# Optimization experiments

Hardware: AMD Instinct MI355X
Metric: run time of the kernel (lower is better)

## Reference

```python
import jax, jax.numpy as jnp
import numpy as np
import math

F_DIM = 256      # feature_dims
NHEADS = 4
KEY_D = 64
VAL_D = 64
ITERS = 6        # update_iters
N_ATOMS = 100000
N_BONDS = 200000
NEI = 6
ATOM_FDIM = 31
BOND_FDIM = 37   # 31 + 6
NEG_SLOPE = 0.1


def setup_inputs() -> dict:
    key = jax.random.key(0)
    ks = jax.random.split(key, 13)
    s = 0.05
    return {
        "fatoms": jax.random.normal(ks[0], (N_ATOMS, ATOM_FDIM), jnp.float32),
        "fbonds": jax.random.normal(ks[1], (N_BONDS, BOND_FDIM), jnp.float32),
        "agraph": jax.random.randint(ks[2], (N_ATOMS, NEI), 0, N_BONDS),
        "bgraph": jax.random.randint(ks[3], (N_BONDS, NEI), 0, N_BONDS),
        "lig_scope": jax.random.randint(ks[4], (64, 2), 0, N_ATOMS),
        "W_emb": jax.random.normal(ks[5], (BOND_FDIM, F_DIM), jnp.float32) * s,
        "b_emb": jnp.zeros((F_DIM,), jnp.float32),
        "Wq": jax.random.normal(ks[6], (F_DIM, NHEADS * KEY_D), jnp.float32) * s,
        "Wk": jax.random.normal(ks[7], (F_DIM, NHEADS * KEY_D), jnp.float32) * s,
        "Wv": jax.random.normal(ks[8], (F_DIM, NHEADS * VAL_D), jnp.float32) * s,
        "Wout": jax.random.normal(ks[9], (VAL_D, F_DIM), jnp.float32) * s,
        "W_last": jax.random.normal(ks[10], (ATOM_FDIM + F_DIM, F_DIM), jnp.float32) * s,
        "b_last": jnp.zeros((F_DIM,), jnp.float32),
    }


def reference(fatoms, fbonds, agraph, bgraph, lig_scope,
              W_emb, b_emb, Wq, Wk, Wv, Wout, W_last, b_last):
    # Bond embedding + initial message
    fbonds_input = fbonds @ W_emb + b_emb                      # [B, F]
    message = jax.nn.leaky_relu(fbonds_input, NEG_SLOPE)
    # index 0 is the padding bond -> masked out in attention
    nei_mask = jnp.where(bgraph != 0, 0.0, -1e7)[:, None, :]   # [B, 1, NEI]
    inv_sqrt_kd = 1.0 / math.sqrt(KEY_D)

    for _ in range(ITERS - 1):
        nei = message[bgraph]                                  # [B, NEI, F] gather
        q = (message @ Wq).reshape(N_BONDS, NHEADS, KEY_D)     # [B, H, K]
        k = (nei @ Wk).reshape(N_BONDS, NEI, NHEADS, KEY_D)    # [B, NEI, H, K]
        v = (nei @ Wv).reshape(N_BONDS, NEI, NHEADS, VAL_D)    # [B, NEI, H, V]
        scores = jnp.einsum('bhk,bnhk->bhn', q, k) * inv_sqrt_kd + nei_mask
        attn = jax.nn.softmax(scores, axis=-1)                 # [B, H, NEI]
        out = jnp.einsum('bhn,bnhv->bhv', attn, v)             # [B, H, V]
        out = out.mean(axis=1)                                 # mean over heads -> [B, V]
        message = jax.nn.leaky_relu(fbonds_input + out @ Wout, NEG_SLOPE)

    # Aggregate incoming bond messages per atom (index 0 acts as padding row)
    nei_sum = message[agraph].sum(axis=1)                      # [A, F]
    h = jnp.concatenate([fatoms, nei_sum], axis=-1) @ W_last + b_last
    return jax.nn.leaky_relu(h, NEG_SLOPE)
```

## Files before the change

kernel.cpp:

```cpp
#include <hip/hip_runtime.h>

#define N_ATOMS 100000
#define N_BONDS 200000
#define NEI 6
#define ITERS 6

#define MB_PAD 200064
#define MT_B 1563
#define MT_Q 3126
#define MT_A 782
#define KL 320
#define KVSTRIDE 768
#define QSTR 260
#define AUX_NT 2

typedef __bf16 bf16x8 __attribute__((ext_vector_type(8)));
typedef float f32x4 __attribute__((ext_vector_type(4)));
typedef float f32x2 __attribute__((ext_vector_type(2)));

__device__ __forceinline__ float b2f(unsigned short u) {
  union { unsigned int i; float f; } x; x.i = ((unsigned int)u) << 16; return x.f;
}
__device__ __forceinline__ unsigned short f2b(float f) {
  union { float f; unsigned int i; } x; x.f = f;
  unsigned int r = (x.i + 0x7FFFu + ((x.i >> 16) & 1u)) >> 16;
  return (unsigned short)r;
}
__device__ __forceinline__ float lrelu(float v) { return v > 0.f ? v : 0.1f * v; }

#if defined(__has_builtin)
#  if __has_builtin(__builtin_amdgcn_cvt_f32_fp8) && __has_builtin(__builtin_amdgcn_cvt_pk_fp8_f32)
#    define HW_FP8 1
#  endif
#  if __has_builtin(__builtin_amdgcn_cvt_pk_f32_fp8)
#    define HW_PKFP8 1
#  endif
#endif

__device__ __forceinline__ unsigned char f2e4m3_sw(float f) {
  union { float f; unsigned u; } x; x.f = f;
  unsigned s = (x.u >> 24) & 0x80u;
  unsigned ax = x.u & 0x7FFFFFFFu;
  if (ax >= 0x43E00000u) return (unsigned char)(s | 0x7Eu);
  if (ax < 0x3A800000u)  return (unsigned char)s;
  if (ax < 0x3C800000u) {
    union { unsigned u; float f; } a; a.u = ax;
    unsigned n = (unsigned)(a.f * 512.0f + 0.5f);
    return (unsigned char)(s | n);
  }
  unsigned r = ax + 0x0007FFFFu + ((ax >> 20) & 1u);
  unsigned e32 = r >> 23;
  unsigned mant = (r >> 20) & 7u;
  int e8 = (int)e32 - 120;
  if (e8 >= 16) return (unsigned char)(s | 0x7Eu);
  return (unsigned char)(s | ((unsigned)e8 << 3) | mant);
}
__device__ __forceinline__ float dec8_sw(unsigned b) {
  unsigned s = (b & 0x80u) << 24;
  unsigned e = (b >> 3) & 0xFu, m = b & 7u;
  if (e) { union { unsigned u; float f; } x; x.u = s | ((e + 120u) << 23) | (m << 20); return x.f; }
  float v = (float)m * 0.001953125f;
  return (b & 0x80u) ? -v : v;
}
#ifdef HW_FP8
__device__ __forceinline__ unsigned char f2e4m3(float f) {
  return (unsigned char)(__builtin_amdgcn_cvt_pk_fp8_f32(f, f, 0, false) & 0xFF);
}
#define DEC0(x) __builtin_amdgcn_cvt_f32_fp8((int)(x), 0)
#define DEC1(x) __builtin_amdgcn_cvt_f32_fp8((int)(x), 1)
#define DEC2(x) __builtin_amdgcn_cvt_f32_fp8((int)(x), 2)
#define DEC3(x) __builtin_amdgcn_cvt_f32_fp8((int)(x), 3)
#else
__device__ __forceinline__ unsigned char f2e4m3(float f) { return f2e4m3_sw(f); }
#define DEC0(x) dec8_sw((x) & 0xFFu)
#define DEC1(x) dec8_sw(((x) >> 8) & 0xFFu)
#define DEC2(x) dec8_sw(((x) >> 16) & 0xFFu)
#define DEC3(x) dec8_sw(((x) >> 24) & 0xFFu)
#endif

__device__ __forceinline__ int kswz(int k, int n) {
  return (k & ~63) | ((k & 63) ^ ((n & 7) << 3));
}

__global__ __launch_bounds__(256) void pack_weights(
    const float* __restrict__ Wq, const float* __restrict__ Wk,
    const float* __restrict__ Wv, const float* __restrict__ Wemb,
    const float* __restrict__ Wout, const float* __restrict__ Wlast,
    unsigned short* __restrict__ wkvT, unsigned short* __restrict__ wqT,
    unsigned short* __restrict__ wmsgT, unsigned short* __restrict__ wlastT)
{
  int t = blockIdx.x * 256 + threadIdx.x;
  {
    int n = t >> 8, k = t & 255;
    wkvT[n * 256 + kswz(k, n)] =
        f2b((n < 256) ? Wk[k * 256 + n] : Wv[k * 256 + (n - 256)]);
  }
  if (t < 65536) {
    int n = t >> 8, k = t & 255;
    wqT[n * 256 + kswz(k, n)] = f2b(Wq[k * 256 + n]);
  }
  if (t < 32768) {
    int n = t >> 7, k = t & 127;
    float v = 0.f;
    if (k < 64)       v = Wout[k * 256 + n];
    else if (k < 101) v = Wemb[(k - 64) * 256 + n];
    wmsgT[n * 128 + kswz(k, n)] = f2b(v);
  }
  if (t < 256 * KL) {
    int n = t / KL, k = t % KL;
    float v = 0.f;
    if (k < 256)      v = Wlast[(31 + k) * 256 + n];
    else if (k < 287) v = Wlast[(k - 256) * 256 + n];
    wlastT[n * KL + kswz(k, n)] = f2b(v);
  }
}

__global__ __launch_bounds__(256) void pack_bonds(
    const float* __restrict__ fbonds, unsigned short* __restrict__ A2)
{
  int t = blockIdx.x * 256 + threadIdx.x;
  int r = t >> 7, c = t & 127;
  float v = 0.f;
  if (c >= 64 && c < 101 && r < N_BONDS) v = fbonds[r * 37 + (c - 64)];
  A2[t] = f2b(v);
}

template<int EP>
__global__ __launch_bounds__(256) void gemm_bt(
    const unsigned short* __restrict__ A,
    const unsigned short* __restrict__ BT,
    unsigned short* __restrict__ C0,
    float* __restrict__ Fout,
    const float* __restrict__ Xf,
    int K, int N, int Mreal)
{
  __shared__ __align__(16) unsigned short As[128 * 64];
  __shared__ __align__(16) unsigned short Bs[128 * 64];
  const int tid  = threadIdx.x;
  const int wave = tid >> 6, lane = tid & 63;
  const int wr = wave >> 1, wc = wave & 1;
  const int lhi = lane >> 4, llo = lane & 15;
  const int mBase = blockIdx.y * 128;
  const int nBase = blockIdx.x * 128;
  const int crow = tid >> 3, ccol = tid & 7;

  f32x4 acc[4][4];
  #pragma unroll
  for (int i = 0; i < 4; ++i)
    #pragma unroll
    for (int j = 0; j < 4; ++j)
      acc[i][j] = f32x4{0.f, 0.f, 0.f, 0.f};

  for (int k0 = 0; k0 < K; k0 += 64) {
    __syncthreads();
    #pragma unroll
    for (int r = 0; r < 4; ++r) {
      const unsigned short* ga =
          A + (size_t)(mBase + r * 32 + crow) * K + (k0 + ccol * 8);
      __builtin_amdgcn_global_load_lds(
          (const __attribute__((address_space(1))) void*)ga,
          (__attribute__((address_space(3))) void*)(As + r * 2048 + wave * 512), 16, 0, 0);
      const unsigned short* gb =
          BT + (size_t)(nBase + r * 32 + crow) * K + (k0 + ccol * 8);
      __builtin_amdgcn_global_load_lds(
          (const __attribute__((address_space(1))) void*)gb,
          (__attribute__((address_space(3))) void*)(Bs + r * 2048 + wave * 512), 16, 0, 0);
    }
    __syncthreads();
    #pragma unroll
    for (int ks = 0; ks < 2; ++ks) {
      bf16x8 af[4], bfv[4];
      #pragma unroll
      for (int i = 0; i < 4; ++i)
        af[i] = *reinterpret_cast<const bf16x8*>(&As[(wr * 64 + i * 16 + llo) * 64 + ks * 32 + lhi * 8]);
      #pragma unroll
      for (int j = 0; j < 4; ++j)
        bfv[j] = *reinterpret_cast<const bf16x8*>(
            &Bs[(wc * 64 + j * 16 + llo) * 64 + ((ks * 32 + lhi * 8) ^ ((llo & 7) << 3))]);
      #pragma unroll
      for (int i = 0; i < 4; ++i)
        #pragma unroll
        for (int j = 0; j < 4; ++j)
          acc[i][j] = __builtin_amdgcn_mfma_f32_16x16x32_bf16(af[i], bfv[j], acc[i][j], 0, 0, 0);
    }
  }

  #pragma unroll
  for (int i = 0; i < 4; ++i) {
    #pragma unroll
    for (int j = 0; j < 4; ++j) {
      const int col = nBase + wc * 64 + j * 16 + llo;
      #pragma unroll
      for (int r = 0; r < 4; ++r) {
        const int row = mBase + wr * 64 + i * 16 + lhi * 4 + r;
        const float v = acc[i][j][r];
        if (EP == 0) {
          C0[(size_t)row * N + col] = f2b(v);
        } else if (EP == 1) {
          C0[(size_t)row * N + col] = f2b(lrelu(v + Xf[col]));
        } else if (EP == 3) {
          if (row < Mreal) Fout[(size_t)row * N + col] = lrelu(v + Xf[col]);
        } else {
          unsigned char* kvb = (unsigned char*)C0;
          if (nBase < 256) {
            kvb[(size_t)row * KVSTRIDE + col] = f2e4m3(v);
          } else {
            *(unsigned short*)(kvb + (size_t)row * KVSTRIDE + 256 +
                               (size_t)(col - 256) * 2) = f2b(v);
          }
        }
      }
    }
  }
}

#ifdef HW_PKFP8
#define QKDOT(p_, kd_) do {                                                    \
    const f32x2 lo_ = __builtin_amdgcn_cvt_pk_f32_fp8((int)(kd_), false);      \
    const f32x2 hi_ = __builtin_amdgcn_cvt_pk_f32_fp8((int)(kd_), true);       \
    p_ = q0 * lo_.x + q1 * lo_.y + q2 * hi_.x + q3 * hi_.y;                    \
  } while (0)
#else
#define QKDOT(p_, kd_) do {                                                    \
    p_ = q0 * DEC0(kd_) + q1 * DEC1(kd_) + q2 * DEC2(kd_) + q3 * DEC3(kd_);    \
  } while (0)
#endif

#define NLOAD(P, N_)                                                           \
    const int bn##P##N_ = __builtin_amdgcn_readfirstlane(                      \
        bgraph[(size_t)uw##P * NEI + N_]);                                     \
    const unsigned char* bp##P##N_ =                                           \
        kv + (size_t)(unsigned)bn##P##N_ * KVSTRIDE;                           \
    const unsigned kd##P##N_ =                                                 \
        *reinterpret_cast<const unsigned*>(bp##P##N_ + lane * 4);              \
    const ushort4 vu##P##N_ =                                                  \
        *reinterpret_cast<const ushort4*>(bp##P##N_ + 256 + lane * 8);

#define GATHER(P, BL)                                                          \
    const int bl##P = (BL);                                                    \
    const int uw##P = __builtin_amdgcn_readfirstlane(mBase + bl##P);           \
    NLOAD(P, 0) NLOAD(P, 1) NLOAD(P, 2) NLOAD(P, 3) NLOAD(P, 4) NLOAD(P, 5)

#define NSCORE(P, N_)                                                          \
    float sc##P##N_;                                                           \
    {                                                                          \
      float p_;                                                                \
      QKDOT(p_, kd##P##N_);                                                    \
      p_ += __shfl_xor(p_, 1); p_ += __shfl_xor(p_, 2);                        \
      p_ += __shfl_xor(p_, 4); p_ += __shfl_xor(p_, 8);                        \
      sc##P##N_ = p_ * SCL + (bn##P##N_ != 0 ? 0.f : -1e7f);                   \
    }

#define NPV(P, N_)                                                             \
    {                                                                          \
      const float e_ = exp2f(sc##P##N_ - m_);                                  \
      s_ += e_;                                                                \
      o0_ += e_ * b2f(vu##P##N_.x); o1_ += e_ * b2f(vu##P##N_.y);              \
      o2_ += e_ * b2f(vu##P##N_.z); o3_ += e_ * b2f(vu##P##N_.w);              \
    }

#define COMPUTE(P)                                                             \
    {                                                                          \
      const ushort4 qu_ = *reinterpret_cast<const ushort4*>(                   \
          &smem[bl##P * QSTR + lane * 4]);                                     \
      const float q0 = b2f(qu_.x), q1 = b2f(qu_.y);                            \
      const float q2 = b2f(qu_.z), q3 = b2f(qu_.w);                            \
      NSCORE(P, 0) NSCORE(P, 1) NSCORE(P, 2)                                   \
      NSCORE(P, 3) NSCORE(P, 4) NSCORE(P, 5)                                   \
      const float m_ =                                                         \
          fmaxf(fmaxf(fmaxf(sc##P##0, sc##P##1), fmaxf(sc##P##2, sc##P##3)),   \
                fmaxf(sc##P##4, sc##P##5));                                    \
      float s_ = 0.f, o0_ = 0.f, o1_ = 0.f, o2_ = 0.f, o3_ = 0.f;              \
      NPV(P, 0) NPV(P, 1) NPV(P, 2) NPV(P, 3) NPV(P, 4) NPV(P, 5)              \
      const float inv_ = 0.25f * __builtin_amdgcn_rcpf(s_);                    \
      o0_ *= inv_; o1_ *= inv_; o2_ *= inv_; o3_ *= inv_;                      \
      o0_ += __shfl_xor(o0_, 16); o0_ += __shfl_xor(o0_, 32);                  \
      o1_ += __shfl_xor(o1_, 16); o1_ += __shfl_xor(o1_, 32);                  \
      o2_ += __shfl_xor(o2_, 16); o2_ += __shfl_xor(o2_, 32);                  \
      o3_ += __shfl_xor(o3_, 16); o3_ += __shfl_xor(o3_, 32);                  \
      if (lane < 16) {                                                         \
        ushort4 ov_;                                                           \
        ov_.x = f2b(o0_); ov_.y = f2b(o1_);                                    \
        ov_.z = f2b(o2_); ov_.w = f2b(o3_);                                    \
        *reinterpret_cast<ushort4*>(                                           \
            A2 + (size_t)(mBase + bl##P) * 128 + lane * 4) = ov_;              \
      }                                                                        \
    }

__global__ __launch_bounds__(512, 6) void fused_qattn(
    const unsigned short* __restrict__ msg,
    const unsigned short* __restrict__ wqT,
    const unsigned char* __restrict__ kv,
    const int* __restrict__ bgraph,
    unsigned short* __restrict__ A2)
{
  __shared__ __align__(16) unsigned short smem[20480];
  const int tid  = threadIdx.x;
  const int wave = tid >> 6, lane = tid & 63;
  const int wr = wave >> 2, wc = wave & 3;
  const int lhi = lane >> 4, llo = lane & 15;
  const int mBase = blockIdx.x * 64;
  const int crow = tid >> 3, ccol = tid & 7;

  f32x4 acc[2][4];
  #pragma unroll
  for (int i = 0; i < 2; ++i)
    #pragma unroll
    for (int j = 0; j < 4; ++j)
      acc[i][j] = f32x4{0.f, 0.f, 0.f, 0.f};

  for (int k0 = 0; k0 < 256; k0 += 64) {
    __syncthreads();
    {
      const unsigned short* ga =
          msg + (size_t)(mBase + crow) * 256 + (k0 + ccol * 8);
      __builtin_amdgcn_global_load_lds(
          (const __attribute__((address_space(1))) void*)ga,
          (__attribute__((address_space(3))) void*)(smem + wave * 512), 16, 0, AUX_NT);
    }
    #pragma unroll
    for (int r = 0; r < 4; ++r) {
      const unsigned short* gb =
          wqT + (size_t)(r * 64 + crow) * 256 + (k0 + ccol * 8);
      __builtin_amdgcn_global_load_lds(
          (const __attribute__((address_space(1))) void*)gb,
          (__attribute__((address_space(3))) void*)(smem + 4096 + r * 4096 + wave * 512),
          16, 0, 0);
    }
    __syncthreads();
    #pragma unroll
    for (int ks = 0; ks < 2; ++ks) {
      bf16x8 af[2], bfv[4];
      #pragma unroll
      for (int i = 0; i < 2; ++i)
        af[i] = *reinterpret_cast<const bf16x8*>(
            &smem[(wr * 32 + i * 16 + llo) * 64 + ks * 32 + lhi * 8]);
      #pragma unroll
      for (int j = 0; j < 4; ++j)
        bfv[j] = *reinterpret_cast<const bf16x8*>(
            &smem[4096 + (wc * 64 + j * 16 + llo) * 64 +
                  ((ks * 32 + lhi * 8) ^ ((llo & 7) << 3))]);
      #pragma unroll
      for (int i = 0; i < 2; ++i)
        #pragma unroll
        for (int j = 0; j < 4; ++j)
          acc[i][j] = __builtin_amdgcn_mfma_f32_16x16x32_bf16(af[i], bfv[j], acc[i][j], 0, 0, 0);
    }
  }
  __syncthreads();

  #pragma unroll
  for (int i = 0; i < 2; ++i) {
    #pragma unroll
    for (int j = 0; j < 4; ++j) {
      const int col = wc * 64 + j * 16 + llo;
      #pragma unroll
      for (int r = 0; r < 4; ++r) {
        const int row = wr * 32 + i * 16 + lhi * 4 + r;
        smem[row * QSTR + col] = f2b(acc[i][j][r]);
      }
    }
  }
  __syncthreads();

  const float SCL = 0.125f * 1.44269504089f;
  const int b0 = wave * 8;
  const int nv = N_BONDS - (mBase + b0);
  if (nv >= 8) {
    { GATHER(A, b0 + 0) GATHER(B, b0 + 1) COMPUTE(A) COMPUTE(B) }
    { GATHER(A, b0 + 2) GATHER(B, b0 + 3) COMPUTE(A) COMPUTE(B) }
    { GATHER(A, b0 + 4) GATHER(B, b0 + 5) COMPUTE(A) COMPUTE(B) }
    { GATHER(A, b0 + 6) GATHER(B, b0 + 7) COMPUTE(A) COMPUTE(B) }
  } else if (nv > 0) {
    #pragma unroll 1
    for (int t2 = 0; t2 < nv; ++t2) { GATHER(A, b0 + t2) COMPUTE(A) }
  }
}

__global__ __launch_bounds__(256) void atom_gather(
    const unsigned short* __restrict__ msg,
    const int* __restrict__ agraph,
    const float* __restrict__ fatoms,
    unsigned short* __restrict__ apad)
{
  const int aid  = blockIdx.x * 4 + (threadIdx.x >> 6);
  const int lane = threadIdx.x & 63;
  if (aid >= N_ATOMS) return;
  float s0 = 0, s1 = 0, s2 = 0, s3 = 0;
  #pragma unroll
  for (int n = 0; n < NEI; ++n) {
    const int b = agraph[aid * NEI + n];
    const ushort4 u = *reinterpret_cast<const ushort4*>(msg + (size_t)b * 256 + lane * 4);
    s0 += b2f(u.x); s1 += b2f(u.y); s2 += b2f(u.z); s3 += b2f(u.w);
  }
  ushort4 ov; ov.x = f2b(s0); ov.y = f2b(s1); ov.z = f2b(s2); ov.w = f2b(s3);
  *reinterpret_cast<ushort4*>(apad + (size_t)aid * KL + lane * 4) = ov;
  apad[(size_t)aid * KL + 256 + lane] =
      (lane < 31) ? f2b(fatoms[(size_t)aid * 31 + lane]) : (unsigned short)0;
}

__global__ __launch_bounds__(256) void diag_out(float* out, int n, float code) {
  int t = blockIdx.x * 256 + threadIdx.x;
  if (t < n) out[t] = (t == 0) ? code : 0.f;
}

extern "C" void kernel_launch(void* const* d_in, const int* in_sizes, int n_in,
                              void* d_out, int out_size, void* d_ws, size_t ws_size,
                              hipStream_t stream) {
  const float* fatoms = (const float*)d_in[0];
  const float* fbonds = (const float*)d_in[1];
  const int* agraph   = (const int*)d_in[2];
  const int* bgraph   = (const int*)d_in[3];
  const float* Wemb   = (const float*)d_in[5];
  const float* bemb   = (const float*)d_in[6];
  const float* Wq     = (const float*)d_in[7];
  const float* Wk     = (const float*)d_in[8];
  const float* Wv     = (const float*)d_in[9];
  const float* Wout   = (const float*)d_in[10];
  const float* Wlast  = (const float*)d_in[11];
  const float* blast  = (const float*)d_in[12];
  float* out          = (float*)d_out;

  char* ws = (char*)d_ws;
  size_t off = 0;
  auto alloc = [&](size_t bytes) {
    char* p = ws + off; off += (bytes + 511) & ~(size_t)511; return p;
  };
  unsigned short* msg    = (unsigned short*)alloc((size_t)MB_PAD * 256 * 2);
  unsigned char*  kv     = (unsigned char*)alloc((size_t)MB_PAD * KVSTRIDE);
  unsigned short* A2     = (unsigned short*)alloc((size_t)MB_PAD * 128 * 2);
  unsigned short* wkvT   = (unsigned short*)alloc((size_t)512 * 256 * 2);
  unsigned short* wqT    = (unsigned short*)alloc((size_t)256 * 256 * 2);
  unsigned short* wmsgT  = (unsigned short*)alloc((size_t)256 * 128 * 2);
  unsigned short* wlastT = (unsigned short*)alloc((size_t)256 * KL * 2);
  unsigned short* apad   = (unsigned short*)kv;

  if (off > ws_size) {
    diag_out<<<dim3((out_size + 255) / 256), dim3(256), 0, stream>>>(
        out, out_size, 10000.f + (float)(ws_size >> 20));
    return;
  }

  pack_weights<<<dim3(512), dim3(256), 0, stream>>>(
      Wq, Wk, Wv, Wemb, Wout, Wlast, wkvT, wqT, wmsgT, wlastT);
  pack_bonds<<<dim3(MB_PAD * 128 / 256), dim3(256), 0, stream>>>(fbonds, A2);

  gemm_bt<1><<<dim3(2, MT_B), dim3(256), 0, stream>>>(
      A2, wmsgT, msg, (float*)nullptr, bemb, 128, 256, MB_PAD);

  for (int it = 0; it < ITERS - 1; ++it) {
    gemm_bt<4><<<dim3(4, MT_B), dim3(256), 0, stream>>>(
        msg, wkvT, (unsigned short*)kv, (float*)nullptr, (const float*)nullptr,
        256, 512, MB_PAD);
    fused_qattn<<<dim3(MT_Q), dim3(512), 0, stream>>>(msg, wqT, kv, bgraph, A2);
    gemm_bt<1><<<dim3(2, MT_B), dim3(256), 0, stream>>>(
        A2, wmsgT, msg, (float*)nullptr, bemb, 128, 256, MB_PAD);
  }

  atom_gather<<<dim3(N_ATOMS / 4), dim3(256), 0, stream>>>(msg, agraph, fatoms, apad);
  gemm_bt<3><<<dim3(2, MT_A), dim3(256), 0, stream>>>(
      apad, wlastT, (unsigned short*)nullptr, out, blast, KL, 256, N_ATOMS);
}
```

Before: 1.856 ms.

## Fuse message output GEMM into attention kernel and write messages in place

Stages the per-bond attention output in shared memory instead of writing it to global A2. The kernel then performs the [attn | fbonds] × Wmsg GEMM with bias and leaky ReLU inside the same block and writes the new message directly. This removes the separate gemm_bt launch per iteration and the global round trip of the attention output. In exchange the kernel uses more shared memory per block, drops the padding on the Q staging stride (which can cause bank conflicts), and writes the result as scattered 2-byte stores into the same msg buffer it reads from.

```diff
diff --git a/kernel.cpp b/kernel.cpp
--- a/kernel.cpp
+++ b/kernel.cpp
@@ -11,7 +11,8 @@
 #define MT_A 782
 #define KL 320
 #define KVSTRIDE 768
-#define QSTR 260
+#define QSTR 256
+#define ATT_OFF 16384
 #define AUX_NT 2
 
 typedef __bf16 bf16x8 __attribute__((ext_vector_type(8)));
@@ -283,16 +284,19 @@
         ov_.x = f2b(o0_); ov_.y = f2b(o1_);                                    \
         ov_.z = f2b(o2_); ov_.w = f2b(o3_);                                    \
         *reinterpret_cast<ushort4*>(                                           \
-            A2 + (size_t)(mBase + bl##P) * 128 + lane * 4) = ov_;              \
+            &smem[ATT_OFF + bl##P * 64 + lane * 4]) = ov_;                     \
       }                                                                        \
     }
 
 __global__ __launch_bounds__(512, 6) void fused_qattn(
-    const unsigned short* __restrict__ msg,
+    const unsigned short* msg,
     const unsigned short* __restrict__ wqT,
     const unsigned char* __restrict__ kv,
     const int* __restrict__ bgraph,
-    unsigned short* __restrict__ A2)
+    const unsigned short* __restrict__ A2,
+    const unsigned short* __restrict__ wmsgT,
+    const float* __restrict__ bemb,
+    unsigned short* msgOut)
 {
   __shared__ __align__(16) unsigned short smem[20480];
   const int tid  = threadIdx.x;
@@ -371,9 +375,79 @@
     { GATHER(A, b0 + 2) GATHER(B, b0 + 3) COMPUTE(A) COMPUTE(B) }
     { GATHER(A, b0 + 4) GATHER(B, b0 + 5) COMPUTE(A) COMPUTE(B) }
     { GATHER(A, b0 + 6) GATHER(B, b0 + 7) COMPUTE(A) COMPUTE(B) }
-  } else if (nv > 0) {
+  } else {
     #pragma unroll 1
-    for (int t2 = 0; t2 < nv; ++t2) { GATHER(A, b0 + t2) COMPUTE(A) }
+    for (int t2 = 0; t2 < 8; ++t2) {
+      if (t2 < nv) {
+        GATHER(A, b0 + t2) COMPUTE(A)
+      } else if (lane < 16) {
+        ushort4 z_; z_.x = 0; z_.y = 0; z_.z = 0; z_.w = 0;
+        *reinterpret_cast<ushort4*>(
+            &smem[ATT_OFF + (b0 + t2) * 64 + lane * 4]) = z_;
+      }
+    }
+  }
+
+  f32x4 acc3[2][2];
+  #pragma unroll 1
+  for (int nh = 0; nh < 2; ++nh) {
+    #pragma unroll
+    for (int i = 0; i < 2; ++i)
+      #pragma unroll
+      for (int j = 0; j < 2; ++j)
+        acc3[i][j] = f32x4{0.f, 0.f, 0.f, 0.f};
+    #pragma unroll 1
+    for (int k0 = 0; k0 < 128; k0 += 64) {
+      __syncthreads();
+      if (nh == 0 && k0 == 0) {
+        const unsigned short* gf =
+            A2 + (size_t)(mBase + crow) * 128 + (64 + ccol * 8);
+        __builtin_amdgcn_global_load_lds(
+            (const __attribute__((address_space(1))) void*)gf,
+            (__attribute__((address_space(3))) void*)(smem + wave * 512), 16, 0, 0);
+      }
+      #pragma unroll
+      for (int r = 0; r < 2; ++r) {
+        const unsigned short* gb =
+            wmsgT + (size_t)(nh * 128 + r * 64 + crow) * 128 + (k0 + ccol * 8);
+        __builtin_amdgcn_global_load_lds(
+            (const __attribute__((address_space(1))) void*)gb,
+            (__attribute__((address_space(3))) void*)(smem + 4096 + r * 4096 + wave * 512),
+            16, 0, 0);
+      }
+      __syncthreads();
+      const int abase = (k0 == 0) ? ATT_OFF : 0;
+      #pragma unroll
+      for (int ks = 0; ks < 2; ++ks) {
+        bf16x8 af3[2], bfv3[2];
+        #pragma unroll
+        for (int i = 0; i < 2; ++i)
+          af3[i] = *reinterpret_cast<const bf16x8*>(
+              &smem[abase + (wr * 32 + i * 16 + llo) * 64 + ks * 32 + lhi * 8]);
+        #pragma unroll
+        for (int j = 0; j < 2; ++j)
+          bfv3[j] = *reinterpret_cast<const bf16x8*>(
+              &smem[4096 + (wc * 32 + j * 16 + llo) * 64 +
+                    ((ks * 32 + lhi * 8) ^ ((llo & 7) << 3))]);
+        #pragma unroll
+        for (int i = 0; i < 2; ++i)
+          #pragma unroll
+          for (int j = 0; j < 2; ++j)
+            acc3[i][j] = __builtin_amdgcn_mfma_f32_16x16x32_bf16(af3[i], bfv3[j], acc3[i][j], 0, 0, 0);
+      }
+    }
+    #pragma unroll
+    for (int i = 0; i < 2; ++i) {
+      #pragma unroll
+      for (int j = 0; j < 2; ++j) {
+        const int col = nh * 128 + wc * 32 + j * 16 + llo;
+        #pragma unroll
+        for (int r = 0; r < 4; ++r) {
+          const int row = mBase + wr * 32 + i * 16 + lhi * 4 + r;
+          msgOut[(size_t)row * 256 + col] = f2b(lrelu(acc3[i][j][r] + bemb[col]));
+        }
+      }
+    }
   }
 }
 
@@ -452,9 +526,8 @@
     gemm_bt<4><<<dim3(4, MT_B), dim3(256), 0, stream>>>(
         msg, wkvT, (unsigned short*)kv, (float*)nullptr, (const float*)nullptr,
         256, 512, MB_PAD);
-    fused_qattn<<<dim3(MT_Q), dim3(512), 0, stream>>>(msg, wqT, kv, bgraph, A2);
-    gemm_bt<1><<<dim3(2, MT_B), dim3(256), 0, stream>>>(
-        A2, wmsgT, msg, (float*)nullptr, bemb, 128, 256, MB_PAD);
+    fused_qattn<<<dim3(MT_Q), dim3(512), 0, stream>>>(
+        msg, wqT, kv, bgraph, A2, wmsgT, bemb, msg);
   }
 
   atom_gather<<<dim3(N_ATOMS / 4), dim3(256), 0, stream>>>(msg, agraph, fatoms, apad);
```

After: 1.939 ms. 1.04x slower.
